# Kernel optimization log

Measured on AMD Instinct MI355X. Metric: run time of the kernel, lower is better.

Reference implementation:

```python
import jax, jax.numpy as jnp
import numpy as np

MARGIN = 5.0  # margin_between_clusters


def setup_inputs() -> dict:
    key = jax.random.key(0)
    k1, k2, k3 = jax.random.split(key, 3)
    N, D, K = 262144, 128, 64
    embeddings = jax.random.normal(k1, (N, D), dtype=jnp.float32)
    cluster_labels = jax.random.randint(k2, (N,), 0, K, dtype=jnp.int64)
    centroids = jax.random.normal(k3, (K, D), dtype=jnp.float32)
    return {"embeddings": embeddings, "cluster_labels": cluster_labels, "centroids": centroids}


def reference(embeddings, cluster_labels, centroids):
    # Assumes all K clusters are present in cluster_labels (true w.h.p. for N >> K),
    # matching number_cluster = len(unique(labels)) in the original.
    N, d = embeddings.shape
    K = centroids.shape[0]
    labels = cluster_labels.astype(jnp.int32)

    x2 = jnp.sum(embeddings * embeddings, axis=1, keepdims=True)        # [N,1]
    c2 = jnp.sum(centroids * centroids, axis=1)[None, :]                # [1,K]
    d2 = jnp.maximum(x2 + c2 - 2.0 * (embeddings @ centroids.T), 0.0)  # [N,K]
    dist = jnp.sqrt(d2)

    rows = jnp.arange(N)
    own_d = dist[rows, labels]                 # distance to own centroid
    counts = jax.ops.segment_sum(jnp.ones((N,), embeddings.dtype), labels, num_segments=K)
    safe_counts = jnp.maximum(counts, 1.0)

    # attraction: per cluster, mean of squared distance to own centroid
    attr_per_cluster = jax.ops.segment_sum(own_d * own_d, labels, num_segments=K) / safe_counts
    attraction_loss = jnp.sum(jnp.where(counts > 0, attr_per_cluster, 0.0))

    # repulsion: per cluster, mean over (points_in_cluster x other_centroids) of relu((m - d)^2)
    rep = jax.nn.relu((MARGIN - dist) ** 2)    # [N,K]
    row_other = (jnp.sum(rep, axis=1) - rep[rows, labels]) / (K - 1)
    rep_per_cluster = jax.ops.segment_sum(row_other, labels, num_segments=K) / safe_counts
    repulsion_loss = jnp.sum(jnp.where(counts > 0, rep_per_cluster, 0.0))

    return (attraction_loss + repulsion_loss) / K
```

## Files before the change

### kernel.cpp

```cpp
#include <hip/hip_runtime.h>


constexpr int N = 262144;
constexpr int D = 128;
constexpr int K = 64;

constexpr int GRID = 768;
constexpr int NWAVES = 4;
constexpr int NWTOT = GRID * NWAVES;
constexpr int NTILES = N / 32;
constexpr int PANEL = 34 * 32;

typedef __bf16 bf16x4 __attribute__((ext_vector_type(4)));
typedef __bf16 bf16x8 __attribute__((ext_vector_type(8)));
typedef float  f32x16 __attribute__((ext_vector_type(16)));

__global__ __launch_bounds__(256, 3) void dcl_main(
    const float* __restrict__ emb,
    const int*   __restrict__ labels,
    const float* __restrict__ cent,
    float* __restrict__ g_attr,
    float* __restrict__ g_rep,
    int*   __restrict__ g_cnt)
{
    __shared__ bf16x8 sA[2 * 8 * 64];
    __shared__ __align__(16) bf16x4 sPanel[NWAVES * PANEL];
    __shared__ float  s_c2[K];
    __shared__ __align__(16) float sC2i0[2][16];
    __shared__ __align__(16) float sC2i1[2][16];
    __shared__ float  s_attr[K];
    __shared__ float  s_rep[K];
    __shared__ int    s_cnt[K];

    const int tid  = threadIdx.x;
    const int wave = tid >> 6;
    const int lane = tid & 63;
    const int l31  = lane & 31;
    const int h    = lane >> 5;

    const int g = blockIdx.x * NWAVES + wave;
    int tiles[3];
    tiles[0] = g;
    tiles[1] = g + NWTOT;
    int nt = 2;
    if (g % 3 != 2) { tiles[2] = 2 * NWTOT + (g - g / 3); nt = 3; }

    float4 buf[16];
    {
        const float4* src = (const float4*)emb + (size_t)tiles[0] * 1024 + lane;
        #pragma unroll
        for (int q = 0; q < 16; ++q) buf[q] = src[q * 64];
    }
    int lbl[3];
    lbl[0] = labels[tiles[0] * 32 + l31];
    lbl[1] = labels[tiles[1] * 32 + l31];
    lbl[2] = (nt == 3) ? labels[tiles[2] * 32 + l31] : 0;

    #pragma unroll
    for (int e = tid; e < 2 * 8 * 64; e += 256) {
        const int t = e >> 9, s = (e >> 6) & 7, l = e & 63;
        const int c  = t * 32 + (l & 31);
        const int d0 = 16 * s + 8 * (l >> 5);
        const float4 f0 = *(const float4*)(cent + c * D + d0);
        const float4 f1 = *(const float4*)(cent + c * D + d0 + 4);
        bf16x8 v;
        v[0] = (__bf16)f0.x; v[1] = (__bf16)f0.y; v[2] = (__bf16)f0.z; v[3] = (__bf16)f0.w;
        v[4] = (__bf16)f1.x; v[5] = (__bf16)f1.y; v[6] = (__bf16)f1.z; v[7] = (__bf16)f1.w;
        sA[e] = v;
    }
    if (tid < K) {
        const float4* cp = (const float4*)(cent + tid * D);
        float s = 0.f;
        #pragma unroll
        for (int q = 0; q < D / 4; ++q) {
            const float4 f = cp[q];
            s = fmaf(f.x, f.x, s); s = fmaf(f.y, f.y, s);
            s = fmaf(f.z, f.z, s); s = fmaf(f.w, f.w, s);
        }
        s_c2[tid] = s;
        s_attr[tid] = 0.f; s_rep[tid] = 0.f; s_cnt[tid] = 0;
    }
    __syncthreads();
    if (tid < 32) {
        const int hh = tid >> 4, r = tid & 15;
        const int rb = (r & 3) + 8 * (r >> 2) + 4 * hh;
        sC2i0[hh][r] = -0.5f * s_c2[rb];
        sC2i1[hh][r] = -0.5f * s_c2[rb + 32];
    }
    __syncthreads();

    bf16x4* panel = sPanel + wave * PANEL;

    for (int i = 0; i < nt; ++i) {
        #pragma unroll
        for (int q = 0; q < 16; ++q) {
            bf16x4 v;
            v[0] = (__bf16)buf[q].x; v[1] = (__bf16)buf[q].y;
            v[2] = (__bf16)buf[q].z; v[3] = (__bf16)buf[q].w;
            const int n = 2 * q + h;
            panel[34 * n + l31] = v;
        }

        if (i + 1 < nt) {
            const float4* src = (const float4*)emb + (size_t)tiles[i + 1] * 1024 + lane;
            #pragma unroll
            for (int q = 0; q < 16; ++q) buf[q] = src[q * 64];
        }

        f32x16 acc0, acc1;
        {
            const float4* p0 = (const float4*)&sC2i0[h][0];
            const float4* p1 = (const float4*)&sC2i1[h][0];
            #pragma unroll
            for (int w = 0; w < 4; ++w) {
                ((float4*)&acc0)[w] = p0[w];
                ((float4*)&acc1)[w] = p1[w];
            }
        }
        float x2p = 0.f;

        #pragma unroll
        for (int s = 0; s < 8; ++s) {
            const bf16x8 b = *(const bf16x8*)&panel[34 * l31 + 4 * s + 2 * h];
            #pragma unroll
            for (int e = 0; e < 8; ++e) {
                const float fe = (float)b[e];
                x2p = fmaf(fe, fe, x2p);
            }
            const bf16x8 a0 = sA[s * 64 + lane];
            const bf16x8 a1 = sA[(8 + s) * 64 + lane];
            acc0 = __builtin_amdgcn_mfma_f32_32x32x16_bf16(a0, b, acc0, 0, 0, 0);
            acc1 = __builtin_amdgcn_mfma_f32_32x32x16_bf16(a1, b, acc1, 0, 0, 0);
        }

        const float x2 = x2p + __shfl_xor(x2p, 32);
        const int li = lbl[i];

        float s1 = 0.f, s2 = 0.f, own = 0.f;
        #pragma unroll
        for (int r = 0; r < 16; ++r) {
            const int rbase = (r & 3) + 8 * (r >> 2) + 4 * h;
            {
                float d2 = fmaf(-2.f, acc0[r], x2);
                d2 = fmaxf(d2, 0.f);
                const float dd = __builtin_amdgcn_sqrtf(d2);
                s1 += dd; s2 += d2;
                if (rbase == li) own += d2;
            }
            {
                float d2 = fmaf(-2.f, acc1[r], x2);
                d2 = fmaxf(d2, 0.f);
                const float dd = __builtin_amdgcn_sqrtf(d2);
                s1 += dd; s2 += d2;
                if (rbase + 32 == li) own += d2;
            }
        }
        s1  += __shfl_xor(s1, 32);
        s2  += __shfl_xor(s2, 32);
        own += __shfl_xor(own, 32);

        if (lane < 32) {
            const float down = __builtin_amdgcn_sqrtf(own);
            const float own_term = fmaf(-10.f, down, 25.f) + own;
            const float row_other = (25.f * K - 10.f * s1 + s2 - own_term) * (1.f / (K - 1));
            atomicAdd(&s_attr[li], own);
            atomicAdd(&s_rep[li], row_other);
            atomicAdd(&s_cnt[li], 1);
        }
    }

    __syncthreads();
    if (tid < K) {
        atomicAdd(&g_attr[tid], s_attr[tid]);
        atomicAdd(&g_rep[tid], s_rep[tid]);
        atomicAdd(&g_cnt[tid], s_cnt[tid]);
    }
}

__global__ void dcl_finish(const float* __restrict__ g_attr,
                           const float* __restrict__ g_rep,
                           const int*   __restrict__ g_cnt,
                           float* __restrict__ out)
{
    const int k = threadIdx.x;
    const float cnt = (float)g_cnt[k];
    float v = (cnt > 0.f) ? (g_attr[k] + g_rep[k]) / cnt : 0.f;
    #pragma unroll
    for (int off = 32; off > 0; off >>= 1) v += __shfl_down(v, off);
    if (k == 0) out[0] = v * (1.f / K);
}

extern "C" void kernel_launch(void* const* d_in, const int* in_sizes, int n_in,
                              void* d_out, int out_size, void* d_ws, size_t ws_size,
                              hipStream_t stream) {
    const float* emb    = (const float*)d_in[0];
    const int*   labels = (const int*)d_in[1];
    const float* cent   = (const float*)d_in[2];
    float* out = (float*)d_out;

    float* g_attr = (float*)d_ws;
    float* g_rep  = g_attr + K;
    int*   g_cnt  = (int*)(g_rep + K);

    hipMemsetAsync(d_ws, 0, 3 * K * sizeof(float), stream);
    dcl_main<<<GRID, 256, 0, stream>>>(emb, labels, cent, g_attr, g_rep, g_cnt);
    dcl_finish<<<1, 64, 0, stream>>>(g_attr, g_rep, g_cnt, out);
}
```

Measured before the change: 235.5 us.

## Use one tile per wave with 2048 blocks and replicated global accumulators

Replaces the persistent 768-block grid, which looped over 2-3 tiles per wave with register prefetch of the next tile, with a 2048-block grid where each wave processes exactly one 32-row tile. Global atomics are spread across 8 replicated accumulator slots, indexed by block, to reduce contention, and the finish kernel sums the replicas. It also splits several reductions into two independent accumulators for more ILP and drops the occupancy hint from launch bounds. The cost is losing the cross-tile prefetch overlap and repeating the per-block centroid staging across many more blocks.

```diff
diff --git a/kernel.cpp b/kernel.cpp
--- a/kernel.cpp
+++ b/kernel.cpp
@@ -5,17 +5,14 @@
 constexpr int D = 128;
 constexpr int K = 64;
 
-constexpr int GRID = 768;
-constexpr int NWAVES = 4;
-constexpr int NWTOT = GRID * NWAVES;
-constexpr int NTILES = N / 32;
+constexpr int GRID = 2048;
 constexpr int PANEL = 34 * 32;
 
 typedef __bf16 bf16x4 __attribute__((ext_vector_type(4)));
 typedef __bf16 bf16x8 __attribute__((ext_vector_type(8)));
 typedef float  f32x16 __attribute__((ext_vector_type(16)));
 
-__global__ __launch_bounds__(256, 3) void dcl_main(
+__global__ __launch_bounds__(256) void dcl_main(
     const float* __restrict__ emb,
     const int*   __restrict__ labels,
     const float* __restrict__ cent,
@@ -24,7 +21,7 @@
     int*   __restrict__ g_cnt)
 {
     __shared__ bf16x8 sA[2 * 8 * 64];
-    __shared__ __align__(16) bf16x4 sPanel[NWAVES * PANEL];
+    __shared__ __align__(16) bf16x4 sPanel[4 * PANEL];
     __shared__ float  s_c2[K];
     __shared__ __align__(16) float sC2i0[2][16];
     __shared__ __align__(16) float sC2i1[2][16];
@@ -38,23 +35,15 @@
     const int l31  = lane & 31;
     const int h    = lane >> 5;
 
-    const int g = blockIdx.x * NWAVES + wave;
-    int tiles[3];
-    tiles[0] = g;
-    tiles[1] = g + NWTOT;
-    int nt = 2;
-    if (g % 3 != 2) { tiles[2] = 2 * NWTOT + (g - g / 3); nt = 3; }
+    const int tile = blockIdx.x * 4 + wave;
 
     float4 buf[16];
     {
-        const float4* src = (const float4*)emb + (size_t)tiles[0] * 1024 + lane;
+        const float4* src = (const float4*)emb + (size_t)tile * 1024 + lane;
         #pragma unroll
         for (int q = 0; q < 16; ++q) buf[q] = src[q * 64];
     }
-    int lbl[3];
-    lbl[0] = labels[tiles[0] * 32 + l31];
-    lbl[1] = labels[tiles[1] * 32 + l31];
-    lbl[2] = (nt == 3) ? labels[tiles[2] * 32 + l31] : 0;
+    const int lbl = labels[tile * 32 + l31];
 
     #pragma unroll
     for (int e = tid; e < 2 * 8 * 64; e += 256) {
@@ -70,14 +59,17 @@
     }
     if (tid < K) {
         const float4* cp = (const float4*)(cent + tid * D);
-        float s = 0.f;
+        float sa = 0.f, sb = 0.f;
         #pragma unroll
-        for (int q = 0; q < D / 4; ++q) {
-            const float4 f = cp[q];
-            s = fmaf(f.x, f.x, s); s = fmaf(f.y, f.y, s);
-            s = fmaf(f.z, f.z, s); s = fmaf(f.w, f.w, s);
-        }
-        s_c2[tid] = s;
+        for (int q = 0; q < D / 8; ++q) {
+            const float4 f = cp[2 * q];
+            const float4 g = cp[2 * q + 1];
+            sa = fmaf(f.x, f.x, sa); sa = fmaf(f.y, f.y, sa);
+            sa = fmaf(f.z, f.z, sa); sa = fmaf(f.w, f.w, sa);
+            sb = fmaf(g.x, g.x, sb); sb = fmaf(g.y, g.y, sb);
+            sb = fmaf(g.z, g.z, sb); sb = fmaf(g.w, g.w, sb);
+        }
+        s_c2[tid] = sa + sb;
         s_attr[tid] = 0.f; s_rep[tid] = 0.f; s_cnt[tid] = 0;
     }
     __syncthreads();
@@ -91,89 +83,85 @@
 
     bf16x4* panel = sPanel + wave * PANEL;
 
-    for (int i = 0; i < nt; ++i) {
+    #pragma unroll
+    for (int q = 0; q < 16; ++q) {
+        bf16x4 v;
+        v[0] = (__bf16)buf[q].x; v[1] = (__bf16)buf[q].y;
+        v[2] = (__bf16)buf[q].z; v[3] = (__bf16)buf[q].w;
+        const int n = 2 * q + h;
+        panel[34 * n + l31] = v;
+    }
+
+    f32x16 acc0, acc1;
+    {
+        const float4* p0 = (const float4*)&sC2i0[h][0];
+        const float4* p1 = (const float4*)&sC2i1[h][0];
         #pragma unroll
-        for (int q = 0; q < 16; ++q) {
-            bf16x4 v;
-            v[0] = (__bf16)buf[q].x; v[1] = (__bf16)buf[q].y;
-            v[2] = (__bf16)buf[q].z; v[3] = (__bf16)buf[q].w;
-            const int n = 2 * q + h;
-            panel[34 * n + l31] = v;
-        }
-
-        if (i + 1 < nt) {
-            const float4* src = (const float4*)emb + (size_t)tiles[i + 1] * 1024 + lane;
-            #pragma unroll
-            for (int q = 0; q < 16; ++q) buf[q] = src[q * 64];
-        }
-
-        f32x16 acc0, acc1;
+        for (int w = 0; w < 4; ++w) {
+            ((float4*)&acc0)[w] = p0[w];
+            ((float4*)&acc1)[w] = p1[w];
+        }
+    }
+
+    float x2A = 0.f, x2B = 0.f;
+    #pragma unroll
+    for (int s = 0; s < 8; ++s) {
+        const bf16x8 b = *(const bf16x8*)&panel[34 * l31 + 4 * s + 2 * h];
         {
-            const float4* p0 = (const float4*)&sC2i0[h][0];
-            const float4* p1 = (const float4*)&sC2i1[h][0];
-            #pragma unroll
-            for (int w = 0; w < 4; ++w) {
-                ((float4*)&acc0)[w] = p0[w];
-                ((float4*)&acc1)[w] = p1[w];
-            }
-        }
-        float x2p = 0.f;
-
-        #pragma unroll
-        for (int s = 0; s < 8; ++s) {
-            const bf16x8 b = *(const bf16x8*)&panel[34 * l31 + 4 * s + 2 * h];
-            #pragma unroll
-            for (int e = 0; e < 8; ++e) {
-                const float fe = (float)b[e];
-                x2p = fmaf(fe, fe, x2p);
-            }
-            const bf16x8 a0 = sA[s * 64 + lane];
-            const bf16x8 a1 = sA[(8 + s) * 64 + lane];
-            acc0 = __builtin_amdgcn_mfma_f32_32x32x16_bf16(a0, b, acc0, 0, 0, 0);
-            acc1 = __builtin_amdgcn_mfma_f32_32x32x16_bf16(a1, b, acc1, 0, 0, 0);
-        }
-
-        const float x2 = x2p + __shfl_xor(x2p, 32);
-        const int li = lbl[i];
-
-        float s1 = 0.f, s2 = 0.f, own = 0.f;
-        #pragma unroll
-        for (int r = 0; r < 16; ++r) {
-            const int rbase = (r & 3) + 8 * (r >> 2) + 4 * h;
-            {
-                float d2 = fmaf(-2.f, acc0[r], x2);
-                d2 = fmaxf(d2, 0.f);
-                const float dd = __builtin_amdgcn_sqrtf(d2);
-                s1 += dd; s2 += d2;
-                if (rbase == li) own += d2;
-            }
-            {
-                float d2 = fmaf(-2.f, acc1[r], x2);
-                d2 = fmaxf(d2, 0.f);
-                const float dd = __builtin_amdgcn_sqrtf(d2);
-                s1 += dd; s2 += d2;
-                if (rbase + 32 == li) own += d2;
-            }
-        }
-        s1  += __shfl_xor(s1, 32);
-        s2  += __shfl_xor(s2, 32);
-        own += __shfl_xor(own, 32);
-
-        if (lane < 32) {
-            const float down = __builtin_amdgcn_sqrtf(own);
-            const float own_term = fmaf(-10.f, down, 25.f) + own;
-            const float row_other = (25.f * K - 10.f * s1 + s2 - own_term) * (1.f / (K - 1));
-            atomicAdd(&s_attr[li], own);
-            atomicAdd(&s_rep[li], row_other);
-            atomicAdd(&s_cnt[li], 1);
-        }
+            const float e0 = (float)b[0], e1 = (float)b[1], e2 = (float)b[2], e3 = (float)b[3];
+            const float e4 = (float)b[4], e5 = (float)b[5], e6 = (float)b[6], e7 = (float)b[7];
+            float p0 = e0 * e0; p0 = fmaf(e1, e1, p0); p0 = fmaf(e2, e2, p0); p0 = fmaf(e3, e3, p0);
+            float p1 = e4 * e4; p1 = fmaf(e5, e5, p1); p1 = fmaf(e6, e6, p1); p1 = fmaf(e7, e7, p1);
+            x2A += p0; x2B += p1;
+        }
+        const bf16x8 a0 = sA[s * 64 + lane];
+        const bf16x8 a1 = sA[(8 + s) * 64 + lane];
+        acc0 = __builtin_amdgcn_mfma_f32_32x32x16_bf16(a0, b, acc0, 0, 0, 0);
+        acc1 = __builtin_amdgcn_mfma_f32_32x32x16_bf16(a1, b, acc1, 0, 0, 0);
+    }
+
+    const float x2p = x2A + x2B;
+    const float x2 = x2p + __shfl_xor(x2p, 32);
+
+    float s1a = 0.f, s1b = 0.f, s2a = 0.f, s2b = 0.f, own = 0.f;
+    #pragma unroll
+    for (int r = 0; r < 16; ++r) {
+        const int rbase = (r & 3) + 8 * (r >> 2) + 4 * h;
+        {
+            float d2 = fmaf(-2.f, acc0[r], x2);
+            d2 = fmaxf(d2, 0.f);
+            const float dd = __builtin_amdgcn_sqrtf(d2);
+            s1a += dd; s2a += d2;
+            if (rbase == lbl) own += d2;
+        }
+        {
+            float d2 = fmaf(-2.f, acc1[r], x2);
+            d2 = fmaxf(d2, 0.f);
+            const float dd = __builtin_amdgcn_sqrtf(d2);
+            s1b += dd; s2b += d2;
+            if (rbase + 32 == lbl) own += d2;
+        }
+    }
+    float s1 = s1a + s1b, s2 = s2a + s2b;
+    s1  += __shfl_xor(s1, 32);
+    s2  += __shfl_xor(s2, 32);
+    own += __shfl_xor(own, 32);
+
+    if (lane < 32) {
+        const float down = __builtin_amdgcn_sqrtf(own);
+        const float own_term = fmaf(-10.f, down, 25.f) + own;
+        const float row_other = (25.f * K - 10.f * s1 + s2 - own_term) * (1.f / (K - 1));
+        atomicAdd(&s_attr[lbl], own);
+        atomicAdd(&s_rep[lbl], row_other);
+        atomicAdd(&s_cnt[lbl], 1);
     }
 
     __syncthreads();
     if (tid < K) {
-        atomicAdd(&g_attr[tid], s_attr[tid]);
-        atomicAdd(&g_rep[tid], s_rep[tid]);
-        atomicAdd(&g_cnt[tid], s_cnt[tid]);
+        const int rep8 = (blockIdx.x & 7) * K;
+        atomicAdd(&g_attr[rep8 + tid], s_attr[tid]);
+        atomicAdd(&g_rep[rep8 + tid], s_rep[tid]);
+        atomicAdd(&g_cnt[rep8 + tid], s_cnt[tid]);
     }
 }
 
@@ -183,8 +171,15 @@
                            float* __restrict__ out)
 {
     const int k = threadIdx.x;
-    const float cnt = (float)g_cnt[k];
-    float v = (cnt > 0.f) ? (g_attr[k] + g_rep[k]) / cnt : 0.f;
+    float a = 0.f, r = 0.f;
+    int   c = 0;
+    #pragma unroll
+    for (int j = 0; j < 8; ++j) {
+        a += g_attr[j * K + k];
+        r += g_rep[j * K + k];
+        c += g_cnt[j * K + k];
+    }
+    float v = (c > 0) ? (a + r) / (float)c : 0.f;
     #pragma unroll
     for (int off = 32; off > 0; off >>= 1) v += __shfl_down(v, off);
     if (k == 0) out[0] = v * (1.f / K);
@@ -199,10 +194,10 @@
     float* out = (float*)d_out;
 
     float* g_attr = (float*)d_ws;
-    float* g_rep  = g_attr + K;
-    int*   g_cnt  = (int*)(g_rep + K);
-
-    hipMemsetAsync(d_ws, 0, 3 * K * sizeof(float), stream);
+    float* g_rep  = g_attr + 8 * K;
+    int*   g_cnt  = (int*)(g_rep + 8 * K);
+
+    hipMemsetAsync(d_ws, 0, 3 * 8 * K * sizeof(float), stream);
     dcl_main<<<GRID, 256, 0, stream>>>(emb, labels, cent, g_attr, g_rep, g_cnt);
     dcl_finish<<<1, 64, 0, stream>>>(g_attr, g_rep, g_cnt, out);
 }
```

Result: faster. 209.9 us (-10.9%).
